# Kernel optimization log

Hardware: AMD Instinct MI355X
Metric: run time of the kernel (lower is better)

## Reference

```python
import jax, jax.numpy as jnp
import numpy as np

EPS = 1e-5  # torch BatchNorm1d default eps


def _bn(x, gamma, beta):
    # Training-mode BatchNorm1d: per-batch mean/var (biased), affine.
    mu = jnp.mean(x, axis=0)
    var = jnp.var(x, axis=0)
    return (x - mu) * jax.lax.rsqrt(var + EPS) * gamma + beta


def _trunk(x, layers):
    # For each hidden layer: Tanh(Linear(BatchNorm(x)))
    for (W, b, g, be) in layers:
        x = jnp.tanh(_bn(x, g, be) @ W + b)
    return x


def setup_inputs() -> dict:
    key = jax.random.key(0)
    ks = jax.random.split(key, 16)
    B, N, D = 4096, 8192, 1024
    dims = [D, 1024, 512, 256]
    inp = {
        "x": jax.random.normal(ks[0], (B, D), dtype=jnp.float32),
        "x_n": jax.random.normal(ks[1], (N, D), dtype=jnp.float32),
        "y_n": jax.random.uniform(ks[2], (N, 1), dtype=jnp.float32),
    }
    for i in range(3):
        fan_in, fan_out = dims[i], dims[i + 1]
        bound = 1.0 / np.sqrt(fan_in)
        inp[f"W{i+1}"] = jax.random.uniform(ks[3 + 4 * i], (fan_in, fan_out), minval=-bound, maxval=bound, dtype=jnp.float32)
        inp[f"b{i+1}"] = jax.random.uniform(ks[4 + 4 * i], (fan_out,), minval=-bound, maxval=bound, dtype=jnp.float32)
        inp[f"g{i+1}"] = jnp.ones((fan_in,), dtype=jnp.float32)
        inp[f"beta{i+1}"] = jnp.zeros((fan_in,), dtype=jnp.float32)
    return inp


def reference(x, x_n, y_n,
              W1, b1, g1, beta1,
              W2, b2, g2, beta2,
              W3, b3, g3, beta3):
    layers = [(W1, b1, g1, beta1), (W2, b2, g2, beta2), (W3, b3, g3, beta3)]
    q = _trunk(x, layers)      # [B, 256]
    k = _trunk(x_n, layers)    # [N, 256]
    # l2 similarity: negative squared euclidean distance, via GEMM.
    # sim[i,j] = -||q_i - k_j||^2 = 2 q_i.k_j - ||q_i||^2 - ||k_j||^2
    q2 = jnp.sum(q * q, axis=1, keepdims=True)          # [B,1]
    k2 = jnp.sum(k * k, axis=1)                          # [N]
    sim = 2.0 * (q @ k.T) - q2 - k2[None, :]             # [B,N]
    # x != x_n (different shapes) => train=False, no diagonal masking.
    scores = jax.nn.softmax(sim, axis=1)
    out = jnp.clip(scores @ y_n, 0.0, 1.0)               # [B,1]
    return jnp.squeeze(out, axis=1)                      # [B]
```

## Files before the change

### kernel.cpp

```cpp
#include <hip/hip_runtime.h>
#include <math.h>
#include <stdint.h>


typedef __attribute__((ext_vector_type(8))) _Float16 half8;
typedef __attribute__((ext_vector_type(4))) _Float16 half4;
typedef __attribute__((ext_vector_type(4))) float floatx4;

#define L2E  1.4426950408889634f
#define SCALE2 2.8853901817f

__device__ __forceinline__ float fast_tanh(float x) {
    float ax = fabsf(x);
    float e  = __expf(-2.0f * ax);
    float r  = (1.0f - e) / (1.0f + e);
    return copysignf(r, x);
}
__device__ __forceinline__ void gload16(const void* g, void* l) {
    __builtin_amdgcn_global_load_lds(
        (__attribute__((address_space(1))) void*)(uintptr_t)(g),
        (__attribute__((address_space(3))) void*)(unsigned int)(uintptr_t)(l),
        16, 0, 0);
}

__global__ __launch_bounds__(256) void preamble(
        const float* __restrict__ xn, const float* __restrict__ x,
        _Float16* __restrict__ xnh, _Float16* __restrict__ xh,
        float* __restrict__ cs0, float* __restrict__ cq0,
        float* __restrict__ cs3, float* __restrict__ cq3,
        const float* __restrict__ W0, const float* __restrict__ W1,
        const float* __restrict__ W2,
        _Float16* __restrict__ T0, _Float16* __restrict__ T1,
        _Float16* __restrict__ T2) {
    const int bx = blockIdx.x;
    if (bx < 384) {
        const float* in; _Float16* out; float *cs, *cq; int r0;
        if (bx < 256) { in = xn; out = xnh; cs = cs0; cq = cq0; r0 = bx * 32; }
        else          { in = x;  out = xh;  cs = cs3; cq = cq3; r0 = (bx - 256) * 32; }
        const int c = threadIdx.x * 4;
        float s0 = 0.f, s1 = 0.f, s2 = 0.f, s3 = 0.f;
        float q0 = 0.f, q1 = 0.f, q2 = 0.f, q3 = 0.f;
        for (int r = r0; r < r0 + 32; ++r) {
            float4 v = *(const float4*)&in[(size_t)r * 1024 + c];
            half4 h;
            h[0] = (_Float16)v.x; h[1] = (_Float16)v.y;
            h[2] = (_Float16)v.z; h[3] = (_Float16)v.w;
            *(half4*)&out[(size_t)r * 1024 + c] = h;
            s0 += v.x; q0 += v.x * v.x;
            s1 += v.y; q1 += v.y * v.y;
            s2 += v.z; q2 += v.z * v.z;
            s3 += v.w; q3 += v.w * v.w;
        }
        atomicAdd(&cs[c + 0], s0); atomicAdd(&cq[c + 0], q0);
        atomicAdd(&cs[c + 1], s1); atomicAdd(&cq[c + 1], q1);
        atomicAdd(&cs[c + 2], s2); atomicAdd(&cq[c + 2], q2);
        atomicAdd(&cs[c + 3], s3); atomicAdd(&cq[c + 3], q3);
    } else {
        const float* W; _Float16* WT; int C, F, f0, c0;
        if (bx < 1408) {
            int idx = bx - 384;  W = W0; WT = T0; C = 1024; F = 1024;
            f0 = (idx & 31) * 32; c0 = (idx >> 5) * 32;
        } else if (bx < 1920) {
            int idx = bx - 1408; W = W1; WT = T1; C = 1024; F = 512;
            f0 = (idx & 15) * 32; c0 = (idx >> 4) * 32;
        } else {
            int idx = bx - 1920; W = W2; WT = T2; C = 512;  F = 256;
            f0 = (idx & 7) * 32;  c0 = (idx >> 3) * 32;
        }
        __shared__ float tile[32][33];
        const int tx = threadIdx.x & 31, ty = threadIdx.x >> 5;
#pragma unroll
        for (int i = 0; i < 32; i += 8)
            tile[ty + i][tx] = W[(size_t)(c0 + ty + i) * F + f0 + tx];
        __syncthreads();
#pragma unroll
        for (int i = 0; i < 32; i += 8)
            WT[(size_t)(f0 + ty + i) * C + c0 + tx] = (_Float16)tile[tx][ty + i];
    }
}

template <int BM, int BN>
__global__ __launch_bounds__(256, 4) void gemm_bn_tanh(
        const _Float16* __restrict__ Ak, const _Float16* __restrict__ Aq,
        const _Float16* __restrict__ WT, const float* __restrict__ bias,
        const float* __restrict__ csK, const float* __restrict__ cqK, float invRK,
        const float* __restrict__ csQ, const float* __restrict__ cqQ, float invRQ,
        const float* __restrict__ g, const float* __restrict__ beta,
        _Float16* __restrict__ Yk, _Float16* __restrict__ Yq,
        int K, int F, int smodeK, int smodeQ,
        float* __restrict__ csOutK, float* __restrict__ cqOutK,
        float* __restrict__ csOutQ, float* __restrict__ cqOutQ,
        float* __restrict__ rowsqK) {
    constexpr int TR = BM / 32;
    constexpr int TC = BN / 32;
    __shared__ _Float16 As[BM * 64];
    __shared__ _Float16 Bs[BN * 64];
    __shared__ _Float16 svh[1024], tvh[1024];
    const int tid = threadIdx.x;
    const int wv = tid >> 6, ln = tid & 63;
    const int quad = ln >> 4, l16 = ln & 15;
    const int wr = wv >> 1, wc = wv & 1;

    const int nxk = 8192 / BM;
    const bool isK = (int)blockIdx.x < nxk;
    const _Float16* A  = isK ? Ak : Aq;
    const float* cs = isK ? csK : csQ;
    const float* cq = isK ? cqK : cqQ;
    const float invR = isK ? invRK : invRQ;
    _Float16* Y        = isK ? Yk : Yq;
    const int smode    = isK ? smodeK : smodeQ;
    float* csO = isK ? csOutK : csOutQ;
    float* cqO = isK ? cqOutK : cqOutQ;
    const int i0 = (isK ? blockIdx.x : blockIdx.x - nxk) * BM;
    const int f0 = blockIdx.y * BN;

    const size_t ldb = (size_t)K * 2;
    const char* Abase = (const char*)(A + (size_t)i0 * K);
    const char* Bbase = (const char*)(WT + (size_t)f0 * K);

    auto stageA = [&](int kb) {
#pragma unroll
        for (int it = 0; it < BM / 32; ++it) {
            int seg = it * 256 + tid;
            int row = seg >> 3, p = seg & 7;
            int lcol = (p ^ row) & 7;
            gload16(Abase + (size_t)row * ldb + kb + lcol * 16, (char*)As + seg * 16);
        }
    };
    auto stageB = [&](int kb) {
#pragma unroll
        for (int it = 0; it < BN / 32; ++it) {
            int seg = it * 256 + tid;
            int row = seg >> 3, p = seg & 7;
            int lcol = (p ^ row) & 7;
            gload16(Bbase + (size_t)row * ldb + kb + lcol * 16, (char*)Bs + seg * 16);
        }
    };

    stageA(0);
    stageB(0);
    for (int c = tid; c < K; c += 256) {
        float mean = cs[c] * invR;
        float var  = fmaxf(cq[c] * invR - mean * mean, 0.f);
        float s    = g[c] * rsqrtf(var + 1e-5f);
        svh[c] = (_Float16)s;
        tvh[c] = (_Float16)(beta[c] - mean * s);
    }

    floatx4 acc[TR][TC];
#pragma unroll
    for (int a = 0; a < TR; ++a)
#pragma unroll
        for (int b = 0; b < TC; ++b) acc[a][b] = (floatx4)0.f;

    const int niter = K >> 6;
    for (int it = 0; it < niter; ++it) {
        __syncthreads();
#pragma unroll
        for (int kk = 0; kk < 2; ++kk) {
            const int kc = it * 64 + kk * 32 + quad * 8;
            half8 sv8 = *(const half8*)&svh[kc];
            half8 tv8 = *(const half8*)&tvh[kc];
            half8 af[TR], bf[TC];
#pragma unroll
            for (int t = 0; t < TR; ++t) {
                int ra = wr * (BM / 2) + t * 16 + l16;
                int ca = ((kk * 4 + quad) ^ ra) & 7;
                af[t] = *(const half8*)((const char*)As + ra * 128 + ca * 16);
                af[t] = af[t] * sv8 + tv8;
            }
#pragma unroll
            for (int t = 0; t < TC; ++t) {
                int rb = wc * (BN / 2) + t * 16 + l16;
                int cb = ((kk * 4 + quad) ^ rb) & 7;
                bf[t] = *(const half8*)((const char*)Bs + rb * 128 + cb * 16);
            }
#pragma unroll
            for (int tr = 0; tr < TR; ++tr)
#pragma unroll
                for (int tc = 0; tc < TC; ++tc)
                    acc[tr][tc] = __builtin_amdgcn_mfma_f32_16x16x32_f16(af[tr], bf[tc], acc[tr][tc], 0, 0, 0);
        }
        __syncthreads();
        if (it + 1 < niter) {
            stageA((it + 1) * 128);
            stageB((it + 1) * 128);
        }
    }
#pragma unroll
    for (int tc = 0; tc < TC; ++tc) {
        int f = f0 + wc * (BN / 2) + tc * 16 + l16;
        float bb = bias[f];
#pragma unroll
        for (int tr = 0; tr < TR; ++tr)
#pragma unroll
            for (int r = 0; r < 4; ++r) {
                int row = i0 + wr * (BM / 2) + tr * 16 + quad * 4 + r;
                float v = fast_tanh(acc[tr][tc][r] + bb);
                acc[tr][tc][r] = v;
                Y[(size_t)row * F + f] = (_Float16)v;
            }
    }
    if (smode == 1) {
#pragma unroll
        for (int tc = 0; tc < TC; ++tc) {
            int f = f0 + wc * (BN / 2) + tc * 16 + l16;
            float s = 0.f, q = 0.f;
#pragma unroll
            for (int tr = 0; tr < TR; ++tr)
#pragma unroll
                for (int r = 0; r < 4; ++r) {
                    float v = acc[tr][tc][r];
                    s += v; q += v * v;
                }
            s += __shfl_xor(s, 16); q += __shfl_xor(q, 16);
            s += __shfl_xor(s, 32); q += __shfl_xor(q, 32);
            if (quad == 0) {
                atomicAdd(&csO[f], s);
                atomicAdd(&cqO[f], q);
            }
        }
    } else if (smode == 2) {
#pragma unroll
        for (int tr = 0; tr < TR; ++tr)
#pragma unroll
            for (int r = 0; r < 4; ++r) {
                float rq = 0.f;
#pragma unroll
                for (int tc = 0; tc < TC; ++tc) {
                    float v = acc[tr][tc][r];
                    rq += v * v;
                }
                rq += __shfl_xor(rq, 1); rq += __shfl_xor(rq, 2);
                rq += __shfl_xor(rq, 4); rq += __shfl_xor(rq, 8);
                if (l16 == 0)
                    atomicAdd(&rowsqK[i0 + wr * (BM / 2) + tr * 16 + quad * 4 + r], rq * L2E);
            }
    }
}

__global__ __launch_bounds__(256, 2) void flash_mfma(
        const _Float16* __restrict__ Q, const _Float16* __restrict__ K3,
        const float* __restrict__ k2s, const float* __restrict__ yv,
        float* __restrict__ pm, float* __restrict__ pl, float* __restrict__ po,
        int jlen, int nsplit) {
    __shared__ _Float16 Ts[128 * 256];
    const int tid = threadIdx.x;
    const int wv = tid >> 6, ln = tid & 63;
    const int quad = ln >> 4, l16 = ln & 15;
    const int i0 = blockIdx.x * 128;
    const int jb = blockIdx.y * jlen;
    const int nch = jlen >> 6;

    auto stage64 = [&](const _Float16* src, int bufseg) {
        const char* sb = (const char*)src;
#pragma unroll
        for (int it = 0; it < 8; ++it) {
            int seg = it * 256 + tid;
            int row = seg >> 5, p = seg & 31;
            int lcol = (p & 24) | ((p ^ row) & 7);
            gload16(sb + (size_t)row * 512 + lcol * 16, (char*)Ts + (bufseg + seg) * 16);
        }
    };

    stage64(Q + (size_t)i0 * 256, 0);
    stage64(Q + (size_t)(i0 + 64) * 256, 2048);
    __syncthreads();
    half8 qf[2][8];
#pragma unroll
    for (int tr = 0; tr < 2; ++tr)
#pragma unroll
        for (int k0 = 0; k0 < 8; ++k0) {
            int row = wv * 32 + tr * 16 + l16;
            int c = k0 * 4 + quad;
            int phys = (c & 24) | ((c ^ row) & 7);
            qf[tr][k0] = *(const half8*)((const char*)Ts + row * 512 + phys * 16);
        }
    asm volatile("s_waitcnt lgkmcnt(0)" ::: "memory");
    __syncthreads();

    float mrun[2][4], lrun[2][4], orun[2][4];
#pragma unroll
    for (int tr = 0; tr < 2; ++tr)
#pragma unroll
        for (int r = 0; r < 4; ++r) { mrun[tr][r] = -INFINITY; lrun[tr][r] = 0.f; orun[tr][r] = 0.f; }

    stage64(K3 + (size_t)jb * 256, 0);
    __syncthreads();
    for (int jc = 0; jc < nch; ++jc) {
        const int j0 = jb + jc * 64;
        const int bseg = (jc & 1) * 2048;
        if (jc + 1 < nch) stage64(K3 + (size_t)(j0 + 64) * 256, 2048 - bseg);
        floatx4 acc[2][4];
#pragma unroll
        for (int a = 0; a < 2; ++a)
#pragma unroll
            for (int b = 0; b < 4; ++b) acc[a][b] = (floatx4)0.f;
#pragma unroll
        for (int k0 = 0; k0 < 8; ++k0) {
            half8 kf[4];
#pragma unroll
            for (int tc = 0; tc < 4; ++tc) {
                int row = tc * 16 + l16;
                int c = k0 * 4 + quad;
                int phys = (c & 24) | ((c ^ row) & 7);
                kf[tc] = *(const half8*)((const char*)Ts + bseg * 16 + row * 512 + phys * 16);
            }
#pragma unroll
            for (int tr = 0; tr < 2; ++tr)
#pragma unroll
                for (int tc = 0; tc < 4; ++tc)
                    acc[tr][tc] = __builtin_amdgcn_mfma_f32_16x16x32_f16(qf[tr][k0], kf[tc], acc[tr][tc], 0, 0, 0);
        }
        float k2v[4], yv4[4];
#pragma unroll
        for (int tc = 0; tc < 4; ++tc) {
            int j = j0 + tc * 16 + l16;
            k2v[tc] = k2s[j];
            yv4[tc] = yv[j];
        }
#pragma unroll
        for (int tr = 0; tr < 2; ++tr)
#pragma unroll
            for (int r = 0; r < 4; ++r) {
                float lg[4], mt = -INFINITY;
#pragma unroll
                for (int tc = 0; tc < 4; ++tc) {
                    lg[tc] = SCALE2 * acc[tr][tc][r] - k2v[tc];
                    mt = fmaxf(mt, lg[tc]);
                }
                float mnew = fmaxf(mrun[tr][r], mt);
                float sc = exp2f(mrun[tr][r] - mnew);
                float sp = 0.f, spy = 0.f;
#pragma unroll
                for (int tc = 0; tc < 4; ++tc) {
                    float p = exp2f(lg[tc] - mnew);
                    sp  += p;
                    spy += p * yv4[tc];
                }
                lrun[tr][r] = lrun[tr][r] * sc + sp;
                orun[tr][r] = orun[tr][r] * sc + spy;
                mrun[tr][r] = mnew;
            }
        __syncthreads();
    }
#pragma unroll
    for (int tr = 0; tr < 2; ++tr)
#pragma unroll
        for (int r = 0; r < 4; ++r) {
            float m = mrun[tr][r], l = lrun[tr][r], o = orun[tr][r];
#pragma unroll
            for (int s = 1; s < 16; s <<= 1) {
                float m2 = __shfl_xor(m, s);
                float l2 = __shfl_xor(l, s);
                float o2 = __shfl_xor(o, s);
                float mn = fmaxf(m, m2);
                float a = exp2f(m - mn), b = exp2f(m2 - mn);
                l = l * a + l2 * b;
                o = o * a + o2 * b;
                m = mn;
            }
            if (l16 == 0) {
                int row = i0 + wv * 32 + tr * 16 + quad * 4 + r;
                size_t idx = (size_t)row * nsplit + blockIdx.y;
                pm[idx] = m;
                pl[idx] = l;
                po[idx] = o;
            }
        }
}

__global__ void combine_k(const float* __restrict__ pm, const float* __restrict__ pl,
                          const float* __restrict__ po, float* __restrict__ out,
                          int B, int nsplit) {
    int i = blockIdx.x * blockDim.x + threadIdx.x;
    if (i >= B) return;
    float M = -INFINITY;
    for (int s = 0; s < nsplit; ++s) M = fmaxf(M, pm[(size_t)i * nsplit + s]);
    float L = 0.f, O = 0.f;
    for (int s = 0; s < nsplit; ++s) {
        float w = exp2f(pm[(size_t)i * nsplit + s] - M);
        L += pl[(size_t)i * nsplit + s] * w;
        O += po[(size_t)i * nsplit + s] * w;
    }
    float r = O / L;
    out[i] = fminf(fmaxf(r, 0.f), 1.f);
}

extern "C" void kernel_launch(void* const* d_in, const int* in_sizes, int n_in,
                              void* d_out, int out_size, void* d_ws, size_t ws_size,
                              hipStream_t stream) {
    const float* x   = (const float*)d_in[0];
    const float* x_n = (const float*)d_in[1];
    const float* y_n = (const float*)d_in[2];
    const float* Wm[3]    = {(const float*)d_in[3],  (const float*)d_in[7],  (const float*)d_in[11]};
    const float* bm[3]    = {(const float*)d_in[4],  (const float*)d_in[8],  (const float*)d_in[12]};
    const float* gm[3]    = {(const float*)d_in[5],  (const float*)d_in[9],  (const float*)d_in[13]};
    const float* betam[3] = {(const float*)d_in[6],  (const float*)d_in[10], (const float*)d_in[14]};
    (void)in_sizes; (void)n_in; (void)out_size; (void)ws_size;

    const int B = 4096, N = 8192;
    const int NSPLIT = 16;
    const size_t M1 = 1024 * 1024;

    _Float16* h0 = (_Float16*)d_ws;
    _Float16* h1 = h0 + 8 * M1;
    _Float16* h2 = h1 + 4 * M1;
    _Float16* h3 = h2 + 8 * M1;
    _Float16* WT1 = h3 + 4 * M1;
    _Float16* WT2 = WT1 + M1;
    _Float16* WT3 = WT2 + M1 / 2;
    float* fb = (float*)(WT3 + M1 / 8);
    float* csA[6], *cqA[6];
    for (int i = 0; i < 6; ++i) { csA[i] = fb + i * 2048; cqA[i] = fb + i * 2048 + 1024; }
    float* k2n = fb + 12288;
    const size_t zero_floats = 12288 + 8192;
    float* pm = fb + zero_floats;
    float* pl = pm + (size_t)B * NSPLIT;
    float* po = pl + (size_t)B * NSPLIT;

    _Float16* xnh = h0, *xh = h1;
    _Float16* actAk = h2, *actAq = h3;
    _Float16* actBk = h0, *actBq = h1;
    _Float16* k3 = h2, *q3 = h2 + 2 * M1;

    hipMemsetAsync(fb, 0, zero_floats * sizeof(float), stream);
    preamble<<<2048, 256, 0, stream>>>(x_n, x, xnh, xh,
                                       csA[0], cqA[0], csA[3], cqA[3],
                                       Wm[0], Wm[1], Wm[2], WT1, WT2, WT3);
    const float invRK = 1.0f / (float)N, invRQ = 1.0f / (float)B;

    gemm_bn_tanh<128, 128><<<dim3(96, 8), 256, 0, stream>>>(
        xnh, xh, WT1, bm[0],
        csA[0], cqA[0], invRK, csA[3], cqA[3], invRQ, gm[0], betam[0],
        actAk, actAq, 1024, 1024, 1, 1,
        csA[1], cqA[1], csA[4], cqA[4], nullptr);
    gemm_bn_tanh<128, 64><<<dim3(96, 8), 256, 0, stream>>>(
        actAk, actAq, WT2, bm[1],
        csA[1], cqA[1], invRK, csA[4], cqA[4], invRQ, gm[1], betam[1],
        actBk, actBq, 1024, 512, 1, 1,
        csA[2], cqA[2], csA[5], cqA[5], nullptr);
    gemm_bn_tanh<64, 64><<<dim3(192, 4), 256, 0, stream>>>(
        actBk, actBq, WT3, bm[2],
        csA[2], cqA[2], invRK, csA[5], cqA[5], invRQ, gm[2], betam[2],
        k3, q3, 512, 256, 2, 0,
        nullptr, nullptr, nullptr, nullptr, k2n);

    flash_mfma<<<dim3(B / 128, NSPLIT), 256, 0, stream>>>(
        q3, k3, k2n, y_n, pm, pl, po, N / NSPLIT, NSPLIT);
    combine_k<<<B / 256, 256, 0, stream>>>(pm, pl, po, (float*)d_out, B, NSPLIT);
}
```

Before: 253.2 us.

## Split flash tile into 2x2 wave grid over rows and key columns

```diff
diff --git a/kernel.cpp b/kernel.cpp
--- a/kernel.cpp
+++ b/kernel.cpp
@@ -248,6 +248,7 @@
     const int tid = threadIdx.x;
     const int wv = tid >> 6, ln = tid & 63;
     const int quad = ln >> 4, l16 = ln & 15;
+    const int rg = wv & 1, cg = wv >> 1;
     const int i0 = blockIdx.x * 128;
     const int jb = blockIdx.y * jlen;
     const int nch = jlen >> 6;
@@ -266,12 +267,12 @@
     stage64(Q + (size_t)i0 * 256, 0);
     stage64(Q + (size_t)(i0 + 64) * 256, 2048);
     __syncthreads();
-    half8 qf[2][8];
-#pragma unroll
-    for (int tr = 0; tr < 2; ++tr)
+    half8 qf[4][8];
+#pragma unroll
+    for (int tr = 0; tr < 4; ++tr)
 #pragma unroll
         for (int k0 = 0; k0 < 8; ++k0) {
-            int row = wv * 32 + tr * 16 + l16;
+            int row = rg * 64 + tr * 16 + l16;
             int c = k0 * 4 + quad;
             int phys = (c & 24) | ((c ^ row) & 7);
             qf[tr][k0] = *(const half8*)((const char*)Ts + row * 512 + phys * 16);
@@ -279,9 +280,9 @@
     asm volatile("s_waitcnt lgkmcnt(0)" ::: "memory");
     __syncthreads();
 
-    float mrun[2][4], lrun[2][4], orun[2][4];
-#pragma unroll
-    for (int tr = 0; tr < 2; ++tr)
+    float mrun[4][4], lrun[4][4], orun[4][4];
+#pragma unroll
+    for (int tr = 0; tr < 4; ++tr)
 #pragma unroll
         for (int r = 0; r < 4; ++r) { mrun[tr][r] = -INFINITY; lrun[tr][r] = 0.f; orun[tr][r] = 0.f; }
 
@@ -291,61 +292,54 @@
         const int j0 = jb + jc * 64;
         const int bseg = (jc & 1) * 2048;
         if (jc + 1 < nch) stage64(K3 + (size_t)(j0 + 64) * 256, 2048 - bseg);
-        floatx4 acc[2][4];
-#pragma unroll
-        for (int a = 0; a < 2; ++a)
-#pragma unroll
-            for (int b = 0; b < 4; ++b) acc[a][b] = (floatx4)0.f;
+        floatx4 acc[4][2];
+#pragma unroll
+        for (int a = 0; a < 4; ++a)
+#pragma unroll
+            for (int b = 0; b < 2; ++b) acc[a][b] = (floatx4)0.f;
 #pragma unroll
         for (int k0 = 0; k0 < 8; ++k0) {
-            half8 kf[4];
-#pragma unroll
-            for (int tc = 0; tc < 4; ++tc) {
-                int row = tc * 16 + l16;
+            half8 kf[2];
+#pragma unroll
+            for (int tc = 0; tc < 2; ++tc) {
+                int row = cg * 32 + tc * 16 + l16;
                 int c = k0 * 4 + quad;
                 int phys = (c & 24) | ((c ^ row) & 7);
                 kf[tc] = *(const half8*)((const char*)Ts + bseg * 16 + row * 512 + phys * 16);
             }
 #pragma unroll
-            for (int tr = 0; tr < 2; ++tr)
-#pragma unroll
-                for (int tc = 0; tc < 4; ++tc)
+            for (int tr = 0; tr < 4; ++tr)
+#pragma unroll
+                for (int tc = 0; tc < 2; ++tc)
                     acc[tr][tc] = __builtin_amdgcn_mfma_f32_16x16x32_f16(qf[tr][k0], kf[tc], acc[tr][tc], 0, 0, 0);
         }
-        float k2v[4], yv4[4];
-#pragma unroll
-        for (int tc = 0; tc < 4; ++tc) {
-            int j = j0 + tc * 16 + l16;
+        float k2v[2], yv2[2];
+#pragma unroll
+        for (int tc = 0; tc < 2; ++tc) {
+            int j = j0 + cg * 32 + tc * 16 + l16;
             k2v[tc] = k2s[j];
-            yv4[tc] = yv[j];
-        }
-#pragma unroll
-        for (int tr = 0; tr < 2; ++tr)
+            yv2[tc] = yv[j];
+        }
+#pragma unroll
+        for (int tr = 0; tr < 4; ++tr)
 #pragma unroll
             for (int r = 0; r < 4; ++r) {
-                float lg[4], mt = -INFINITY;
-#pragma unroll
-                for (int tc = 0; tc < 4; ++tc) {
-                    lg[tc] = SCALE2 * acc[tr][tc][r] - k2v[tc];
-                    mt = fmaxf(mt, lg[tc]);
-                }
+                float lg[2];
+                lg[0] = SCALE2 * acc[tr][0][r] - k2v[0];
+                lg[1] = SCALE2 * acc[tr][1][r] - k2v[1];
+                float mt = fmaxf(lg[0], lg[1]);
                 float mnew = fmaxf(mrun[tr][r], mt);
                 float sc = exp2f(mrun[tr][r] - mnew);
-                float sp = 0.f, spy = 0.f;
-#pragma unroll
-                for (int tc = 0; tc < 4; ++tc) {
-                    float p = exp2f(lg[tc] - mnew);
-                    sp  += p;
-                    spy += p * yv4[tc];
-                }
-                lrun[tr][r] = lrun[tr][r] * sc + sp;
-                orun[tr][r] = orun[tr][r] * sc + spy;
+                float p0 = exp2f(lg[0] - mnew);
+                float p1 = exp2f(lg[1] - mnew);
+                lrun[tr][r] = lrun[tr][r] * sc + p0 + p1;
+                orun[tr][r] = orun[tr][r] * sc + p0 * yv2[0] + p1 * yv2[1];
                 mrun[tr][r] = mnew;
             }
         __syncthreads();
     }
 #pragma unroll
-    for (int tr = 0; tr < 2; ++tr)
+    for (int tr = 0; tr < 4; ++tr)
 #pragma unroll
         for (int r = 0; r < 4; ++r) {
             float m = mrun[tr][r], l = lrun[tr][r], o = orun[tr][r];
@@ -360,14 +354,39 @@
                 o = o * a + o2 * b;
                 m = mn;
             }
-            if (l16 == 0) {
-                int row = i0 + wv * 32 + tr * 16 + quad * 4 + r;
-                size_t idx = (size_t)row * nsplit + blockIdx.y;
-                pm[idx] = m;
-                pl[idx] = l;
-                po[idx] = o;
-            }
-        }
+            mrun[tr][r] = m; lrun[tr][r] = l; orun[tr][r] = o;
+        }
+    float* TsF = (float*)Ts;
+    if (cg == 1 && l16 == 0) {
+#pragma unroll
+        for (int tr = 0; tr < 4; ++tr)
+#pragma unroll
+            for (int r = 0; r < 4; ++r) {
+                int row = rg * 64 + tr * 16 + quad * 4 + r;
+                TsF[row]       = mrun[tr][r];
+                TsF[128 + row] = lrun[tr][r];
+                TsF[256 + row] = orun[tr][r];
+            }
+    }
+    __syncthreads();
+    if (cg == 0 && l16 == 0) {
+#pragma unroll
+        for (int tr = 0; tr < 4; ++tr)
+#pragma unroll
+            for (int r = 0; r < 4; ++r) {
+                int row = rg * 64 + tr * 16 + quad * 4 + r;
+                float m2 = TsF[row], l2 = TsF[128 + row], o2 = TsF[256 + row];
+                float m = mrun[tr][r];
+                float mn = fmaxf(m, m2);
+                float a = exp2f(m - mn), b = exp2f(m2 - mn);
+                float L = lrun[tr][r] * a + l2 * b;
+                float O = orun[tr][r] * a + o2 * b;
+                size_t idx = (size_t)(i0 + row) * nsplit + blockIdx.y;
+                pm[idx] = mn;
+                pl[idx] = L;
+                po[idx] = O;
+            }
+    }
 }
 
 __global__ void combine_k(const float* __restrict__ pm, const float* __restrict__ pl,
```

After: 269.3 us. 1.06x slower.
